# Kernel optimization log

Hardware: AMD Instinct MI355X
Metric: run time of the kernel (lower is better)

The kernel has to match this reference:

```python
import jax, jax.numpy as jnp
import numpy as np

B, T, V, C, H, E, O, NL = 2048, 128, 256, 32, 128, 256, 256, 3
BN = E // 8  # bottleneck = 32
G = 3 * H    # stacked gate dim (r,z,n) = 384
LN_EPS = 1e-5


def setup_inputs() -> dict:
    key = jax.random.key(0)
    ks = jax.random.split(key, 19)
    s = 0.1
    return {
        "tokens": jax.random.randint(ks[0], (B, T), 0, V),
        "lang_ids": jax.random.randint(ks[1], (B,), 0, NL),
        "char_embed": jax.random.normal(ks[2], (V, C)) * s,
        "w_ih_f": jax.random.normal(ks[3], (G, C)) * s,
        "w_hh_f": jax.random.normal(ks[4], (G, H)) * s,
        "b_ih_f": jax.random.normal(ks[5], (G,)) * s,
        "b_hh_f": jax.random.normal(ks[6], (G,)) * s,
        "w_ih_b": jax.random.normal(ks[7], (G, C)) * s,
        "w_hh_b": jax.random.normal(ks[8], (G, H)) * s,
        "b_ih_b": jax.random.normal(ks[9], (G,)) * s,
        "b_hh_b": jax.random.normal(ks[10], (G,)) * s,
        "down_w": jax.random.normal(ks[11], (NL, BN, E)) * s,
        "down_b": jax.random.normal(ks[12], (NL, BN)) * s,
        "up_w": jax.random.normal(ks[13], (NL, E, BN)) * s,
        "up_b": jax.random.normal(ks[14], (NL, E)) * s,
        "ln_g": jnp.ones((NL, E)),
        "ln_b": jnp.zeros((NL, E)),
        "proj_w": jax.random.normal(ks[15], (O, E)) * s,
        "proj_b": jax.random.normal(ks[16], (O,)) * s,
    }


def _gru_last_hidden(x, w_ih, w_hh, b_ih, b_hh):
    """x: [B,T,C] -> final hidden [B,H]. torch GRU gate order (r,z,n)."""
    xp = jnp.einsum('btc,gc->btg', x, w_ih) + b_ih        # [B,T,3H]
    xp = jnp.swapaxes(xp, 0, 1)                           # [T,B,3H]
    h0 = jnp.zeros((x.shape[0], w_hh.shape[1]), x.dtype)

    def step(h, xp_t):
        gh = h @ w_hh.T + b_hh
        xr, xz, xn = jnp.split(xp_t, 3, axis=-1)
        hr, hz, hn = jnp.split(gh, 3, axis=-1)
        r = jax.nn.sigmoid(xr + hr)
        z = jax.nn.sigmoid(xz + hz)
        n = jnp.tanh(xn + r * hn)
        return (1.0 - z) * n + z * h, None

    hT, _ = jax.lax.scan(step, h0, xp)
    return hT


def reference(tokens, lang_ids, char_embed,
              w_ih_f, w_hh_f, b_ih_f, b_hh_f,
              w_ih_b, w_hh_b, b_ih_b, b_hh_b,
              down_w, down_b, up_w, up_b, ln_g, ln_b,
              proj_w, proj_b):
    emb = char_embed[tokens]                              # [B,T,C]
    h_f = _gru_last_hidden(emb, w_ih_f, w_hh_f, b_ih_f, b_hh_f)
    h_b = _gru_last_hidden(emb[:, ::-1], w_ih_b, w_hh_b, b_ih_b, b_hh_b)
    feat = jnp.concatenate([h_f, h_b], axis=-1)           # [B,E]

    # per-sample language-routed bottleneck adapter (gathered expert params)
    hid = jax.nn.gelu(
        jnp.einsum('be,bde->bd', feat, down_w[lang_ids]) + down_b[lang_ids],
        approximate=False)                                # [B,BN]
    adapted = jnp.einsum('bd,bed->be', hid, up_w[lang_ids]) + up_b[lang_ids]
    x = feat + adapted
    mu = jnp.mean(x, axis=-1, keepdims=True)
    var = jnp.var(x, axis=-1, keepdims=True)
    xn = (x - mu) / jnp.sqrt(var + LN_EPS)
    y = xn * ln_g[lang_ids] + ln_b[lang_ids]              # [B,E]

    return y @ proj_w.T + proj_b                          # [B,O]
```

## Files before the change

kernel.cpp:

```cpp
#include <hip/hip_runtime.h>
#include <hip/hip_bf16.h>
#include <hip/hip_fp16.h>

#define Bn 2048
#define Tn 128
#define Vn 256
#define Cn 32
#define Hn 128
#define En 256
#define On 256
#define Gn 384
#define BNn 32

typedef _Float16 f16;
typedef __attribute__((ext_vector_type(8))) _Float16 h8;
typedef __attribute__((ext_vector_type(4))) _Float16 h4;
typedef __attribute__((ext_vector_type(4))) float f4;

#define LOG2E 1.4426950408889634f

__device__ __forceinline__ float fexp2(float x) { return __builtin_amdgcn_exp2f(x); }
__device__ __forceinline__ float frcp(float x) { return __builtin_amdgcn_rcpf(x); }

__global__ void build_table_k(const float* __restrict__ emb,
                              const float* __restrict__ wf,
                              const float* __restrict__ bfv,
                              const float* __restrict__ wb,
                              const float* __restrict__ bbv,
                              f16* __restrict__ xt) {
  const int dir = blockIdx.x >> 8;
  const int v = blockIdx.x & 255;
  const int j = threadIdx.x;
  const float* w = dir ? wb : wf;
  const float* bi = dir ? bbv : bfv;
  const float sc[3] = {-LOG2E, -LOG2E, 2.0f * LOG2E};
  h4 o;
  o[3] = (f16)0.f;
#pragma unroll
  for (int ga = 0; ga < 3; ++ga) {
    const int g = ga * Hn + j;
    float acc = bi[g];
    const f4* wr = (const f4*)(w + g * Cn);
    const f4* er = (const f4*)(emb + v * Cn);
#pragma unroll
    for (int q = 0; q < 8; ++q) {
      f4 wv = wr[q], ev = er[q];
      acc = fmaf(ev.x, wv.x, acc);
      acc = fmaf(ev.y, wv.y, acc);
      acc = fmaf(ev.z, wv.z, acc);
      acc = fmaf(ev.w, wv.w, acc);
    }
    o[ga] = (f16)(acc * sc[ga]);
  }
  *(h4*)&xt[((dir * Vn + v) * Hn + j) * 4] = o;
}

__launch_bounds__(512, 2)
__global__ void gru_k(const int* __restrict__ tokens,
                      const float* __restrict__ whhf,
                      const float* __restrict__ bhhf,
                      const float* __restrict__ whhb,
                      const float* __restrict__ bhhb,
                      const f16* __restrict__ xt,
                      float* __restrict__ feat) {
  const int dir = blockIdx.x & 1;
  const int b0 = (blockIdx.x >> 1) * 16;
  const int tid = threadIdx.x;
  const int wv = tid >> 6;
  const int ln = tid & 63;
  const int lr = ln & 15;
  const int lg = ln >> 4;
  const int j0 = wv * 16;
  const int j = j0 + lr;

  __shared__ f16 hfrag[2 * 2048];
  __shared__ int tokl[16 * 128];

  for (int i = tid; i < 16 * 128; i += 512)
    tokl[i] = tokens[(b0 + (i >> 7)) * Tn + (i & 127)];
  for (int i = tid; i < 2 * 2048; i += 512) hfrag[i] = (f16)0.f;

  const float* whh = dir ? whhb : whhf;
  const float* bhh = dir ? bhhb : bhhf;
  const f16* tab = xt + dir * (Vn * Hn * 4);

  const float gsc[3] = {-LOG2E, -LOG2E, 2.0f * LOG2E};
  h8 Bf[3][4];
#pragma unroll
  for (int ga = 0; ga < 3; ++ga) {
    const float* wr = whh + (ga * Hn + j) * Hn + lg * 8;
#pragma unroll
    for (int kk = 0; kk < 4; ++kk) {
      h8 b;
#pragma unroll
      for (int i = 0; i < 8; ++i) b[i] = (f16)(wr[kk * 32 + i] * gsc[ga]);
      Bf[ga][kk] = b;
    }
  }
  const float bh0 = bhh[j] * (-LOG2E);
  const float bh1 = bhh[Hn + j] * (-LOG2E);
  const float bh2 = bhh[2 * Hn + j] * (2.0f * LOG2E);

  __syncthreads();

  const int aoff = lg * 256 + lr * 16;
  const int woff = (j >> 3) * 256 + (j & 7) * 2 + lg * 64;

  h4 xc[4], xn[4];
  {
    const int tt = dir ? (Tn - 1) : 0;
#pragma unroll
    for (int r = 0; r < 4; ++r) {
      const int tok = tokl[(lg * 4 + r) * 128 + tt];
      xc[r] = *(const h4*)(tab + tok * 512 + j * 4);
    }
  }

  float hprev[4] = {0.f, 0.f, 0.f, 0.f};
  int p = 0;

#pragma unroll 1
  for (int t = 0; t < Tn; ++t) {
    const int tn = (t + 1 < Tn) ? (t + 1) : t;
    const int tt2 = dir ? (Tn - 1 - tn) : tn;
#pragma unroll
    for (int r = 0; r < 4; ++r) {
      const int tok = tokl[(lg * 4 + r) * 128 + tt2];
      xn[r] = *(const h4*)(tab + tok * 512 + j * 4);
    }

    const char* hb = (const char*)hfrag + p * 4096;
    f4 aR = {bh0, bh0, bh0, bh0};
    f4 aZ = {bh1, bh1, bh1, bh1};
    f4 aN = {bh2, bh2, bh2, bh2};
#pragma unroll
    for (int kk = 0; kk < 4; ++kk) {
      h8 a = *(const h8*)(hb + kk * 1024 + aoff);
      aR = __builtin_amdgcn_mfma_f32_16x16x32_f16(a, Bf[0][kk], aR, 0, 0, 0);
      aZ = __builtin_amdgcn_mfma_f32_16x16x32_f16(a, Bf[1][kk], aZ, 0, 0, 0);
      aN = __builtin_amdgcn_mfma_f32_16x16x32_f16(a, Bf[2][kk], aN, 0, 0, 0);
    }

#pragma unroll
    for (int r = 0; r < 4; ++r) {
      const h4 xv = xc[r];
      const float rg = frcp(1.0f + fexp2((float)xv[0] + aR[r]));
      const float zg = frcp(1.0f + fexp2((float)xv[1] + aZ[r]));
      const float ng = fmaf(-2.0f, frcp(1.0f + fexp2(fmaf(rg, aN[r], (float)xv[2]))), 1.0f);
      hprev[r] = fmaf(zg, hprev[r] - ng, ng);
    }

    char* hw = (char*)hfrag + (p ^ 1) * 4096;
#pragma unroll
    for (int r = 0; r < 4; ++r)
      *(f16*)(hw + woff + r * 16) = (f16)hprev[r];

#pragma unroll
    for (int r = 0; r < 4; ++r) xc[r] = xn[r];

    asm volatile("s_waitcnt lgkmcnt(0)\n\ts_barrier" ::: "memory");
    p ^= 1;
  }

#pragma unroll
  for (int r = 0; r < 4; ++r)
    feat[(b0 + lg * 4 + r) * En + dir * Hn + j] = hprev[r];
}

__launch_bounds__(256, 2)
__global__ void epi_k(const float* __restrict__ feat,
                      const int* __restrict__ lang_ids,
                      const float* __restrict__ down_w,
                      const float* __restrict__ down_b,
                      const float* __restrict__ up_w,
                      const float* __restrict__ up_b,
                      const float* __restrict__ ln_g,
                      const float* __restrict__ ln_b,
                      const float* __restrict__ proj_w,
                      const float* __restrict__ proj_b,
                      float* __restrict__ out) {
  const int tid = threadIdx.x;
  const int wv = tid >> 6, ln = tid & 63;
  const int b0 = blockIdx.x * 8;

  __shared__ float fl[8][En];
  __shared__ f16 yA[16][En + 8];

#pragma unroll
  for (int s = 0; s < 8; ++s) fl[s][tid] = feat[(b0 + s) * En + tid];
  {
    f16* z = &yA[0][0];
    for (int i = tid; i < 16 * (En + 8); i += 256) z[i] = (f16)0.f;
  }
  __syncthreads();

#pragma unroll 1
  for (int si = 0; si < 2; ++si) {
    const int s = wv * 2 + si;
    const int lang = lang_ids[b0 + s];

    const int d = ln & 31, hf = ln >> 5;
    const f4* dwv = (const f4*)(down_w + (lang * BNn + d) * En + hf * 128);
    const f4* fsv = (const f4*)&fl[s][hf * 128];
    float pacc = 0.f;
#pragma unroll
    for (int q = 0; q < 32; ++q) {
      f4 a = fsv[q], w = dwv[q];
      pacc = fmaf(a.x, w.x, pacc);
      pacc = fmaf(a.y, w.y, pacc);
      pacc = fmaf(a.z, w.z, pacc);
      pacc = fmaf(a.w, w.w, pacc);
    }
    pacc += __shfl_xor(pacc, 32);
    const float hv = pacc + down_b[lang * BNn + d];
    const float hid = 0.5f * hv * (1.0f + erff(hv * 0.70710678118f));

    float hh[32];
#pragma unroll
    for (int dd = 0; dd < 32; ++dd) hh[dd] = __shfl(hid, dd);

    const int e0 = ln * 4;
    float x[4];
    float s1 = 0.f, s2 = 0.f;
#pragma unroll
    for (int i = 0; i < 4; ++i) {
      const f4* ur = (const f4*)(up_w + (lang * En + e0 + i) * BNn);
      float a = 0.f;
#pragma unroll
      for (int q = 0; q < 8; ++q) {
        f4 u = ur[q];
        a = fmaf(hh[q * 4 + 0], u.x, a);
        a = fmaf(hh[q * 4 + 1], u.y, a);
        a = fmaf(hh[q * 4 + 2], u.z, a);
        a = fmaf(hh[q * 4 + 3], u.w, a);
      }
      x[i] = a + fl[s][e0 + i] + up_b[lang * En + e0 + i];
      s1 += x[i];
      s2 = fmaf(x[i], x[i], s2);
    }
#pragma unroll
    for (int off = 32; off >= 1; off >>= 1) {
      s1 += __shfl_xor(s1, off);
      s2 += __shfl_xor(s2, off);
    }
    const float mu = s1 * (1.0f / En);
    const float var = s2 * (1.0f / En) - mu * mu;
    const float rs = rsqrtf(var + 1e-5f);
#pragma unroll
    for (int i = 0; i < 4; ++i) {
      const float yv = (x[i] - mu) * rs * ln_g[lang * En + e0 + i] + ln_b[lang * En + e0 + i];
      yA[s][e0 + i] = (f16)yv;
    }
  }
  __syncthreads();

  const int lr = ln & 15, lg = ln >> 4;
  f4 acc[4];
#pragma unroll
  for (int tt = 0; tt < 4; ++tt) {
    const float pb = proj_b[wv * 64 + tt * 16 + lr];
    acc[tt] = (f4){pb, pb, pb, pb};
  }
#pragma unroll
  for (int kk = 0; kk < 8; ++kk) {
    h8 aF = *(const h8*)(&yA[lr][kk * 32 + lg * 8]);
#pragma unroll
    for (int tt = 0; tt < 4; ++tt) {
      const int o0 = wv * 64 + tt * 16;
      const float* pw = proj_w + (o0 + lr) * En + kk * 32 + lg * 8;
      h8 bF;
#pragma unroll
      for (int i = 0; i < 8; ++i) bF[i] = (f16)pw[i];
      acc[tt] = __builtin_amdgcn_mfma_f32_16x16x32_f16(aF, bF, acc[tt], 0, 0, 0);
    }
  }
  if (lg < 2) {
#pragma unroll
    for (int tt = 0; tt < 4; ++tt) {
      const int o0 = wv * 64 + tt * 16;
#pragma unroll
      for (int r = 0; r < 4; ++r)
        out[(b0 + lg * 4 + r) * On + o0 + lr] = acc[tt][r];
    }
  }
}

extern "C" void kernel_launch(void* const* d_in, const int* in_sizes, int n_in,
                              void* d_out, int out_size, void* d_ws, size_t ws_size,
                              hipStream_t stream) {
  const int* tokens = (const int*)d_in[0];
  const int* lang_ids = (const int*)d_in[1];
  const float* emb = (const float*)d_in[2];
  const float* w_ih_f = (const float*)d_in[3];
  const float* w_hh_f = (const float*)d_in[4];
  const float* b_ih_f = (const float*)d_in[5];
  const float* b_hh_f = (const float*)d_in[6];
  const float* w_ih_b = (const float*)d_in[7];
  const float* w_hh_b = (const float*)d_in[8];
  const float* b_ih_b = (const float*)d_in[9];
  const float* b_hh_b = (const float*)d_in[10];
  const float* down_w = (const float*)d_in[11];
  const float* down_b = (const float*)d_in[12];
  const float* up_w = (const float*)d_in[13];
  const float* up_b = (const float*)d_in[14];
  const float* ln_g = (const float*)d_in[15];
  const float* ln_b = (const float*)d_in[16];
  const float* proj_w = (const float*)d_in[17];
  const float* proj_b = (const float*)d_in[18];

  f16* xt = (f16*)d_ws;
  float* feat = (float*)((char*)d_ws + 2 * Vn * Hn * 4 * 2);

  build_table_k<<<dim3(512), dim3(128), 0, stream>>>(emb, w_ih_f, b_ih_f, w_ih_b, b_ih_b, xt);
  gru_k<<<dim3(256), dim3(512), 0, stream>>>(tokens, w_hh_f, b_hh_f, w_hh_b, b_hh_b, xt, feat);
  epi_k<<<dim3(256), dim3(256), 0, stream>>>(feat, lang_ids, down_w, down_b, up_w, up_b,
                                             ln_g, ln_b, proj_w, proj_b, (float*)d_out);
}
```

Baseline: 131.1 us.

## Restructure GRU recurrence loop: fold biases, fp32 table, swizzled LDS, unroll by two

Folds the r/z recurrent biases into the precomputed input-projection table and stores that table in fp32, removing the per-step bias init and the f16-to-f32 conversions. Tokens are stored time-major and already reversed for the backward direction, so each step reads four tokens with one vector LDS load, prefetched two steps ahead. The hidden-state LDS layout gets an XOR swizzle to reduce bank conflicts. The time loop is manually unrolled by two with register ping-pong, which drops the per-step copies. The fp32 table doubles the gather traffic, and the workspace layout changes to match.

```diff
diff --git a/kernel.cpp b/kernel.cpp
--- a/kernel.cpp
+++ b/kernel.cpp
@@ -14,7 +14,6 @@
 
 typedef _Float16 f16;
 typedef __attribute__((ext_vector_type(8))) _Float16 h8;
-typedef __attribute__((ext_vector_type(4))) _Float16 h4;
 typedef __attribute__((ext_vector_type(4))) float f4;
 
 #define LOG2E 1.4426950408889634f
@@ -24,22 +23,25 @@
 
 __global__ void build_table_k(const float* __restrict__ emb,
                               const float* __restrict__ wf,
-                              const float* __restrict__ bfv,
+                              const float* __restrict__ bif,
+                              const float* __restrict__ bhf,
                               const float* __restrict__ wb,
-                              const float* __restrict__ bbv,
-                              f16* __restrict__ xt) {
+                              const float* __restrict__ bib,
+                              const float* __restrict__ bhb,
+                              float* __restrict__ xt) {
   const int dir = blockIdx.x >> 8;
   const int v = blockIdx.x & 255;
   const int j = threadIdx.x;
   const float* w = dir ? wb : wf;
-  const float* bi = dir ? bbv : bfv;
+  const float* bi = dir ? bib : bif;
+  const float* bh = dir ? bhb : bhf;
   const float sc[3] = {-LOG2E, -LOG2E, 2.0f * LOG2E};
-  h4 o;
-  o[3] = (f16)0.f;
+  f4 o;
+  o[3] = 0.f;
 #pragma unroll
   for (int ga = 0; ga < 3; ++ga) {
     const int g = ga * Hn + j;
-    float acc = bi[g];
+    float acc = bi[g] + (ga < 2 ? bh[g] : 0.f);
     const f4* wr = (const f4*)(w + g * Cn);
     const f4* er = (const f4*)(emb + v * Cn);
 #pragma unroll
@@ -50,9 +52,9 @@
       acc = fmaf(ev.z, wv.z, acc);
       acc = fmaf(ev.w, wv.w, acc);
     }
-    o[ga] = (f16)(acc * sc[ga]);
-  }
-  *(h4*)&xt[((dir * Vn + v) * Hn + j) * 4] = o;
+    o[ga] = acc * sc[ga];
+  }
+  *(f4*)&xt[((dir * Vn + v) * Hn + j) * 4] = o;
 }
 
 __launch_bounds__(512, 2)
@@ -61,7 +63,7 @@
                       const float* __restrict__ bhhf,
                       const float* __restrict__ whhb,
                       const float* __restrict__ bhhb,
-                      const f16* __restrict__ xt,
+                      const float* __restrict__ xt,
                       float* __restrict__ feat) {
   const int dir = blockIdx.x & 1;
   const int b0 = (blockIdx.x >> 1) * 16;
@@ -70,19 +72,20 @@
   const int ln = tid & 63;
   const int lr = ln & 15;
   const int lg = ln >> 4;
-  const int j0 = wv * 16;
-  const int j = j0 + lr;
+  const int j = wv * 16 + lr;
 
   __shared__ f16 hfrag[2 * 2048];
-  __shared__ int tokl[16 * 128];
-
-  for (int i = tid; i < 16 * 128; i += 512)
-    tokl[i] = tokens[(b0 + (i >> 7)) * Tn + (i & 127)];
+  __shared__ int tokT[Tn * 16];
+
+  for (int i = tid; i < Tn * 16; i += 512) {
+    const int t = i >> 4, s = i & 15;
+    tokT[i] = tokens[(b0 + s) * Tn + (dir ? (Tn - 1 - t) : t)];
+  }
   for (int i = tid; i < 2 * 2048; i += 512) hfrag[i] = (f16)0.f;
 
   const float* whh = dir ? whhb : whhf;
   const float* bhh = dir ? bhhb : bhhf;
-  const f16* tab = xt + dir * (Vn * Hn * 4);
+  const char* tab = (const char*)(xt + dir * (Vn * Hn * 4));
 
   const float gsc[3] = {-LOG2E, -LOG2E, 2.0f * LOG2E};
   h8 Bf[3][4];
@@ -97,74 +100,103 @@
       Bf[ga][kk] = b;
     }
   }
-  const float bh0 = bhh[j] * (-LOG2E);
-  const float bh1 = bhh[Hn + j] * (-LOG2E);
-  const float bh2 = bhh[2 * Hn + j] * (2.0f * LOG2E);
+  const float b2 = bhh[2 * Hn + j] * (2.0f * LOG2E);
+  const f4 BH2 = {b2, b2, b2, b2};
+  const f4 Z4 = {0.f, 0.f, 0.f, 0.f};
 
   __syncthreads();
 
-  const int aoff = lg * 256 + lr * 16;
-  const int woff = (j >> 3) * 256 + (j & 7) * 2 + lg * 64;
-
-  h4 xc[4], xn[4];
+  const int aadr = (lg * 256 + lr * 16) ^ ((lg & 1) << 5);
+  int wadr[4];
   {
-    const int tt = dir ? (Tn - 1) : 0;
-#pragma unroll
-    for (int r = 0; r < 4; ++r) {
-      const int tok = tokl[(lg * 4 + r) * 128 + tt];
-      xc[r] = *(const h4*)(tab + tok * 512 + j * 4);
-    }
-  }
-
-  float hprev[4] = {0.f, 0.f, 0.f, 0.f};
-  int p = 0;
+    const int wmask = ((j >> 3) & 1) << 5;
+    const int wbase = (j >> 3) * 256 + (j & 7) * 2 + lg * 64;
+#pragma unroll
+    for (int r = 0; r < 4; ++r) wadr[r] = (wbase + r * 16) ^ wmask;
+  }
+  const int tadr = lg * 16;
+  const int jb = j * 16;
+
+  int4 tkA = *(const int4*)((const char*)tokT + tadr);
+  f4 xc0, xc1, xc2, xc3, xn0, xn1, xn2, xn3;
+  xc0 = *(const f4*)(tab + ((long)tkA.x << 11) + jb);
+  xc1 = *(const f4*)(tab + ((long)tkA.y << 11) + jb);
+  xc2 = *(const f4*)(tab + ((long)tkA.z << 11) + jb);
+  xc3 = *(const f4*)(tab + ((long)tkA.w << 11) + jb);
+  int4 tkB = *(const int4*)((const char*)tokT + 64 + tadr);
+
+  float h0 = 0.f, h1 = 0.f, h2 = 0.f, h3 = 0.f;
+
+#define GRU_BODY(T, P, C0, C1, C2, C3, N0, N1, N2, N3, TKc, TKn)               \
+  {                                                                            \
+    N0 = *(const f4*)(tab + ((long)TKc.x << 11) + jb);                         \
+    N1 = *(const f4*)(tab + ((long)TKc.y << 11) + jb);                         \
+    N2 = *(const f4*)(tab + ((long)TKc.z << 11) + jb);                         \
+    N3 = *(const f4*)(tab + ((long)TKc.w << 11) + jb);                         \
+    {                                                                          \
+      const int tt = ((T) + 2 < Tn) ? ((T) + 2) : (Tn - 1);                    \
+      TKn = *(const int4*)((const char*)tokT + tt * 64 + tadr);                \
+    }                                                                          \
+    const char* hb = (const char*)hfrag + (P) * 4096;                          \
+    h8 A0 = *(const h8*)(hb + aadr + 0 * 1024);                                \
+    h8 A1 = *(const h8*)(hb + aadr + 1 * 1024);                                \
+    h8 A2 = *(const h8*)(hb + aadr + 2 * 1024);                                \
+    h8 A3 = *(const h8*)(hb + aadr + 3 * 1024);                                \
+    f4 aR = __builtin_amdgcn_mfma_f32_16x16x32_f16(A0, Bf[0][0], Z4, 0, 0, 0); \
+    f4 aZ = __builtin_amdgcn_mfma_f32_16x16x32_f16(A0, Bf[1][0], Z4, 0, 0, 0); \
+    f4 aN = __builtin_amdgcn_mfma_f32_16x16x32_f16(A0, Bf[2][0], BH2, 0, 0, 0);\
+    aR = __builtin_amdgcn_mfma_f32_16x16x32_f16(A1, Bf[0][1], aR, 0, 0, 0);    \
+    aZ = __builtin_amdgcn_mfma_f32_16x16x32_f16(A1, Bf[1][1], aZ, 0, 0, 0);    \
+    aN = __builtin_amdgcn_mfma_f32_16x16x32_f16(A1, Bf[2][1], aN, 0, 0, 0);    \
+    aR = __builtin_amdgcn_mfma_f32_16x16x32_f16(A2, Bf[0][2], aR, 0, 0, 0);    \
+    aZ = __builtin_amdgcn_mfma_f32_16x16x32_f16(A2, Bf[1][2], aZ, 0, 0, 0);    \
+    aN = __builtin_amdgcn_mfma_f32_16x16x32_f16(A2, Bf[2][2], aN, 0, 0, 0);    \
+    aR = __builtin_amdgcn_mfma_f32_16x16x32_f16(A3, Bf[0][3], aR, 0, 0, 0);    \
+    aZ = __builtin_amdgcn_mfma_f32_16x16x32_f16(A3, Bf[1][3], aZ, 0, 0, 0);    \
+    aN = __builtin_amdgcn_mfma_f32_16x16x32_f16(A3, Bf[2][3], aN, 0, 0, 0);    \
+    char* hw = (char*)hfrag + ((P) ^ 1) * 4096;                                \
+    {                                                                          \
+      const float rg = frcp(1.f + fexp2(C0.x + aR[0]));                        \
+      const float zg = frcp(1.f + fexp2(C0.y + aZ[0]));                        \
+      const float ng = fmaf(-2.f, frcp(1.f + fexp2(fmaf(rg, aN[0], C0.z))), 1.f); \
+      h0 = fmaf(zg, h0 - ng, ng);                                              \
+      *(f16*)(hw + wadr[0]) = (f16)h0;                                         \
+    }                                                                          \
+    {                                                                          \
+      const float rg = frcp(1.f + fexp2(C1.x + aR[1]));                        \
+      const float zg = frcp(1.f + fexp2(C1.y + aZ[1]));                        \
+      const float ng = fmaf(-2.f, frcp(1.f + fexp2(fmaf(rg, aN[1], C1.z))), 1.f); \
+      h1 = fmaf(zg, h1 - ng, ng);                                              \
+      *(f16*)(hw + wadr[1]) = (f16)h1;                                         \
+    }                                                                          \
+    {                                                                          \
+      const float rg = frcp(1.f + fexp2(C2.x + aR[2]));                        \
+      const float zg = frcp(1.f + fexp2(C2.y + aZ[2]));                        \
+      const float ng = fmaf(-2.f, frcp(1.f + fexp2(fmaf(rg, aN[2], C2.z))), 1.f); \
+      h2 = fmaf(zg, h2 - ng, ng);                                              \
+      *(f16*)(hw + wadr[2]) = (f16)h2;                                         \
+    }                                                                          \
+    {                                                                          \
+      const float rg = frcp(1.f + fexp2(C3.x + aR[3]));                        \
+      const float zg = frcp(1.f + fexp2(C3.y + aZ[3]));                        \
+      const float ng = fmaf(-2.f, frcp(1.f + fexp2(fmaf(rg, aN[3], C3.z))), 1.f); \
+      h3 = fmaf(zg, h3 - ng, ng);                                              \
+      *(f16*)(hw + wadr[3]) = (f16)h3;                                         \
+    }                                                                          \
+    asm volatile("s_waitcnt lgkmcnt(0)\n\ts_barrier" ::: "memory");            \
+  }
 
 #pragma unroll 1
-  for (int t = 0; t < Tn; ++t) {
-    const int tn = (t + 1 < Tn) ? (t + 1) : t;
-    const int tt2 = dir ? (Tn - 1 - tn) : tn;
-#pragma unroll
-    for (int r = 0; r < 4; ++r) {
-      const int tok = tokl[(lg * 4 + r) * 128 + tt2];
-      xn[r] = *(const h4*)(tab + tok * 512 + j * 4);
-    }
-
-    const char* hb = (const char*)hfrag + p * 4096;
-    f4 aR = {bh0, bh0, bh0, bh0};
-    f4 aZ = {bh1, bh1, bh1, bh1};
-    f4 aN = {bh2, bh2, bh2, bh2};
-#pragma unroll
-    for (int kk = 0; kk < 4; ++kk) {
-      h8 a = *(const h8*)(hb + kk * 1024 + aoff);
-      aR = __builtin_amdgcn_mfma_f32_16x16x32_f16(a, Bf[0][kk], aR, 0, 0, 0);
-      aZ = __builtin_amdgcn_mfma_f32_16x16x32_f16(a, Bf[1][kk], aZ, 0, 0, 0);
-      aN = __builtin_amdgcn_mfma_f32_16x16x32_f16(a, Bf[2][kk], aN, 0, 0, 0);
-    }
-
-#pragma unroll
-    for (int r = 0; r < 4; ++r) {
-      const h4 xv = xc[r];
-      const float rg = frcp(1.0f + fexp2((float)xv[0] + aR[r]));
-      const float zg = frcp(1.0f + fexp2((float)xv[1] + aZ[r]));
-      const float ng = fmaf(-2.0f, frcp(1.0f + fexp2(fmaf(rg, aN[r], (float)xv[2]))), 1.0f);
-      hprev[r] = fmaf(zg, hprev[r] - ng, ng);
-    }
-
-    char* hw = (char*)hfrag + (p ^ 1) * 4096;
-#pragma unroll
-    for (int r = 0; r < 4; ++r)
-      *(f16*)(hw + woff + r * 16) = (f16)hprev[r];
-
-#pragma unroll
-    for (int r = 0; r < 4; ++r) xc[r] = xn[r];
-
-    asm volatile("s_waitcnt lgkmcnt(0)\n\ts_barrier" ::: "memory");
-    p ^= 1;
-  }
-
-#pragma unroll
-  for (int r = 0; r < 4; ++r)
-    feat[(b0 + lg * 4 + r) * En + dir * Hn + j] = hprev[r];
+  for (int t = 0; t < Tn; t += 2) {
+    GRU_BODY(t, 0, xc0, xc1, xc2, xc3, xn0, xn1, xn2, xn3, tkB, tkA)
+    GRU_BODY(t + 1, 1, xn0, xn1, xn2, xn3, xc0, xc1, xc2, xc3, tkA, tkB)
+  }
+#undef GRU_BODY
+
+  feat[(b0 + lg * 4 + 0) * En + dir * Hn + j] = h0;
+  feat[(b0 + lg * 4 + 1) * En + dir * Hn + j] = h1;
+  feat[(b0 + lg * 4 + 2) * En + dir * Hn + j] = h2;
+  feat[(b0 + lg * 4 + 3) * En + dir * Hn + j] = h3;
 }
 
 __launch_bounds__(256, 2)
@@ -308,10 +340,11 @@
   const float* proj_w = (const float*)d_in[17];
   const float* proj_b = (const float*)d_in[18];
 
-  f16* xt = (f16*)d_ws;
-  float* feat = (float*)((char*)d_ws + 2 * Vn * Hn * 4 * 2);
-
-  build_table_k<<<dim3(512), dim3(128), 0, stream>>>(emb, w_ih_f, b_ih_f, w_ih_b, b_ih_b, xt);
+  float* xt = (float*)d_ws;
+  float* feat = (float*)((char*)d_ws + 2 * Vn * Hn * 4 * 4);
+
+  build_table_k<<<dim3(512), dim3(128), 0, stream>>>(emb, w_ih_f, b_ih_f, b_hh_f,
+                                                     w_ih_b, b_ih_b, b_hh_b, xt);
   gru_k<<<dim3(256), dim3(512), 0, stream>>>(tokens, w_hh_f, b_hh_f, w_hh_b, b_hh_b, xt, feat);
   epi_k<<<dim3(256), dim3(256), 0, stream>>>(feat, lang_ids, down_w, down_b, up_w, up_b,
                                              ln_g, ln_b, proj_w, proj_b, (float*)d_out);
```

Result: slower. 133.8 us (+2.0%).
